# Performance work log

Measured on AMD Instinct MI355X. Metric: run time of the kernel, lower is better.

Reference implementation:

```python
import jax, jax.numpy as jnp
import numpy as np

B, S, P = 64, 1024, 1024
D_IN, D, OUT = 50, 300, 1024
LN_EPS = 1e-6  # custom LayerNorm in repo-style code (a_2/b_2, eps=1e-6)


def setup_inputs() -> dict:
    key = jax.random.key(0)
    ks = jax.random.split(key, 16)
    std = 1e-4  # matches torch .normal_(mean=0, std=0.0001)
    return {
        "x": jax.random.normal(ks[0], (B, S, D_IN), jnp.float32),
        "matrix_embed": jax.random.normal(ks[1], (D_IN, D), jnp.float32),
        "past": jax.random.normal(ks[2], (B, P, D_IN), jnp.float32),
        "w_pt": jax.random.normal(ks[3], (D_IN, D), jnp.float32) * std,
        "b_pt": jax.random.normal(ks[4], (1, D), jnp.float32) * std,
        "w_pg": jax.random.normal(ks[5], (D_IN, D), jnp.float32) * std,
        "b_pg": jax.random.normal(ks[6], (1, D), jnp.float32) * std,
        "w_ps": jax.random.normal(ks[7], (D_IN, D), jnp.float32) * std,
        "b_ps": jax.random.normal(ks[8], (1, D), jnp.float32) * std,
        "w_ex": jax.random.normal(ks[9], (D_IN, D), jnp.float32) * std,
        "b_ex": jax.random.normal(ks[10], (1, D), jnp.float32) * std,
        "ln_g": jnp.ones((D,), jnp.float32),
        "ln_b": jnp.zeros((D,), jnp.float32),
        "W1": jax.random.normal(ks[11], (D, D), jnp.float32) * 0.05,
        "b1": jnp.zeros((D,), jnp.float32),
        "W2": jax.random.normal(ks[12], (D, OUT), jnp.float32) * 0.05,
        "b2": jnp.zeros((OUT,), jnp.float32),
    }


def _layernorm(h, g, b):
    mu = jnp.mean(h, axis=-1, keepdims=True)
    var = jnp.mean(jnp.square(h - mu), axis=-1, keepdims=True)
    return g * (h - mu) / jnp.sqrt(var + LN_EPS) + b


def reference(x, matrix_embed, past, w_pt, b_pt, w_pg, b_pg, w_ps, b_ps,
              w_ex, b_ex, ln_g, ln_b, W1, b1, W2, b2):
    # token: [B,S,300]
    token = _layernorm(x @ matrix_embed, ln_g, ln_b)
    past_token = jnp.tanh(x @ w_pt + b_pt)          # [B,S,300]
    past_vector = jnp.tanh(past @ w_pg + b_pg)      # [B,P,300]
    past_gate = jax.nn.sigmoid(jnp.einsum('bsd,bpd->bsp', past_token, past_vector))
    past_state = jnp.tanh(past @ w_ps + b_ps)       # [B,P,300]
    pre_state = past_gate @ past_state              # [B,S,300]
    expose_vector = jnp.tanh(x @ w_ex + b_ex)       # [B,S,300]
    expose_gate = jax.nn.sigmoid(jnp.einsum('bsd,btd->bst', expose_vector, pre_state))
    filter_token = token + expose_gate @ pre_state  # [B,S,300]
    # output MLP (dropout is identity in eval mode)
    h = jax.nn.relu(filter_token @ W1 + b1)
    return h @ W2 + b2
```

## Files before the change

kernel.cpp:

```cpp
#include <hip/hip_runtime.h>
#include <hip/hip_bf16.h>
#include <math.h>

typedef __attribute__((ext_vector_type(8))) short bf16x8;
typedef __attribute__((ext_vector_type(4))) float f32x4;

__device__ inline float bf2f(short u) {
  union { float f; unsigned int i; } v;
  v.i = ((unsigned int)(unsigned short)u) << 16;
  return v.f;
}
__device__ inline short f2bf(float f) {
  union { float f; unsigned int i; } v; v.f = f;
  unsigned int r = v.i + 0x7fff + ((v.i >> 16) & 1);
  return (short)(r >> 16);
}

__global__ void pad_rows(const float* __restrict__ src, short* __restrict__ dst,
                         int C, int Cp, int total) {
  int i = blockIdx.x * 256 + threadIdx.x;
  if (i >= total) return;
  int r = i / Cp, c = i - r * Cp;
  dst[i] = f2bf(c < C ? src[(size_t)r * C + c] : 0.f);
}

__global__ void pad_T(const float* __restrict__ src, short* __restrict__ dst,
                      int K, int N, int Kp, int total) {
  int i = blockIdx.x * 256 + threadIdx.x;
  if (i >= total) return;
  int n = i / Kp, k = i - n * Kp;
  dst[i] = f2bf((k < K && n < N) ? src[(size_t)k * N + n] : 0.f);
}

__global__ __launch_bounds__(256) void transpose_pd(const short* __restrict__ in,
                                                    short* __restrict__ out) {
  __shared__ unsigned int T[64][32];
  const int b = blockIdx.z, p0 = blockIdx.x * 64, d0 = blockIdx.y * 64;
  const short* ib = in + (size_t)b * 1024 * 320;
  short* ob = out + (size_t)b * 320 * 1024;
  for (int i = threadIdx.x; i < 512; i += 256) {
    int p = i >> 3, g = i & 7;
    uint4 v = *(const uint4*)&ib[(size_t)(p0 + p) * 320 + d0 + g * 8];
    int s = p & 31;
    T[p][(4 * g + 0) ^ s] = v.x;
    T[p][(4 * g + 1) ^ s] = v.y;
    T[p][(4 * g + 2) ^ s] = v.z;
    T[p][(4 * g + 3) ^ s] = v.w;
  }
  __syncthreads();
  for (int i = threadIdx.x; i < 512; i += 256) {
    int d = i >> 3, g = i & 7;
    int w0 = d >> 1;
    __align__(16) unsigned short tmp[8];
#pragma unroll
    for (int j = 0; j < 8; ++j) {
      int p = g * 8 + j;
      unsigned int val = T[p][w0 ^ (p & 31)];
      tmp[j] = (d & 1) ? (unsigned short)(val >> 16) : (unsigned short)(val & 0xffff);
    }
    *(uint4*)&ob[(size_t)(d0 + d) * 1024 + p0 + g * 8] = *(const uint4*)tmp;
  }
}

template<int NT, int MODE>
__global__ __launch_bounds__(512) void gemm_ep(
    const short* __restrict__ A, const short* __restrict__ Bt, int K,
    const float* __restrict__ bias, int biasN,
    void* __restrict__ outp, int outStride)
{
  __shared__ __align__(16) short Bst[NT][40];
  const int tid = threadIdx.x;
  const int wave = tid >> 6, lane = tid & 63;
  const int m = lane & 15, quad = lane >> 4;
  const int row0 = blockIdx.x * 128 + wave * 16;
  const int n0 = blockIdx.y * NT;

  f32x4 zero = {0.f, 0.f, 0.f, 0.f};
  f32x4 acc[NT / 16];
#pragma unroll
  for (int i = 0; i < NT / 16; ++i) acc[i] = zero;

  const short* arow = A + (size_t)(row0 + m) * K;

  for (int k0 = 0; k0 < K; k0 += 32) {
    __syncthreads();
    for (int idx = tid; idx < NT * 4; idx += 512) {
      int n = idx >> 2, kc = (idx & 3) << 3;
      *(uint4*)&Bst[n][kc] = *(const uint4*)&Bt[(size_t)(n0 + n) * K + k0 + kc];
    }
    __syncthreads();
    bf16x8 af = *(const bf16x8*)(arow + k0 + quad * 8);
#pragma unroll
    for (int nt = 0; nt < NT / 16; ++nt) {
      bf16x8 bf = *(const bf16x8*)&Bst[nt * 16 + m][quad * 8];
      acc[nt] = __builtin_amdgcn_mfma_f32_16x16x32_bf16(af, bf, acc[nt], 0, 0, 0);
    }
  }

#pragma unroll
  for (int nt = 0; nt < NT / 16; ++nt) {
#pragma unroll
    for (int r = 0; r < 4; ++r) {
      int row = row0 + quad * 4 + r;
      int col = n0 + nt * 16 + m;
      float v = acc[nt][r];
      if (MODE != 0) v += (col < biasN) ? bias[col] : 0.f;
      if (MODE == 1) v = tanhf(v);
      if (MODE == 2) v = fmaxf(v, 0.f);
      if (MODE == 3)
        ((float*)outp)[(size_t)row * outStride + col] = v;
      else
        ((short*)outp)[(size_t)row * outStride + col] = f2bf(v);
    }
  }
}

__global__ __launch_bounds__(256) void ln_rows(short* __restrict__ tp,
                                               const float* __restrict__ g,
                                               const float* __restrict__ bb) {
  const int wave = threadIdx.x >> 6, lane = threadIdx.x & 63;
  const int row = blockIdx.x * 4 + wave;
  short* p = tp + (size_t)row * 320;
  float vals[5], s = 0.f, ss = 0.f;
#pragma unroll
  for (int i = 0; i < 5; ++i) {
    int c = lane + i * 64;
    float v = (c < 300) ? bf2f(p[c]) : 0.f;
    vals[i] = v; s += v; ss += v * v;
  }
#pragma unroll
  for (int off = 32; off > 0; off >>= 1) { s += __shfl_down(s, off); ss += __shfl_down(ss, off); }
  s = __shfl(s, 0); ss = __shfl(ss, 0);
  const float mu = s * (1.f / 300.f);
  const float rstd = rsqrtf(ss * (1.f / 300.f) - mu * mu + 1e-6f);
#pragma unroll
  for (int i = 0; i < 5; ++i) {
    int c = lane + i * 64;
    float v = (c < 300) ? (g[c] * (vals[i] - mu) * rstd + bb[c]) : 0.f;
    p[c] = f2bf(v);
  }
}

__global__ __launch_bounds__(512) void attn_v2(
    const short* __restrict__ Qm, const short* __restrict__ Km,
    const short* __restrict__ VT, const short* __restrict__ tokp,
    short* __restrict__ Outp)
{
  __shared__ __align__(16) short Ks[32][328];
  __shared__ __align__(16) short Vt[320][40];
  __shared__ __align__(16) short Ps[8][16][40];
  const int tid = threadIdx.x;
  const int wave = tid >> 6, lane = tid & 63;
  const int m = lane & 15, quad = lane >> 4;
  const int b = blockIdx.x;
  const int qrow0 = b * 1024 + blockIdx.y * 128 + wave * 16;
  const size_t kbase = (size_t)b * 1024 * 320;
  const short* vtb = VT + (size_t)b * 320 * 1024;

  bf16x8 qf[10];
#pragma unroll
  for (int c = 0; c < 10; ++c)
    qf[c] = *(const bf16x8*)&Qm[(size_t)(qrow0 + m) * 320 + c * 32 + quad * 8];

  f32x4 zero = {0.f, 0.f, 0.f, 0.f};
  f32x4 o[20];
#pragma unroll
  for (int i = 0; i < 20; ++i) o[i] = zero;

  for (int pt = 0; pt < 32; ++pt) {
    const int p0 = pt * 32;
    __syncthreads();
    for (int idx = tid; idx < 1280; idx += 512) {
      int p = idx / 40, g = idx - p * 40;
      *(uint4*)&Ks[p][g * 8] = *(const uint4*)&Km[kbase + (size_t)(p0 + p) * 320 + g * 8];
    }
    for (int idx = tid; idx < 1280; idx += 512) {
      int d = idx >> 2, g = idx & 3;
      *(uint4*)&Vt[d][g * 8] = *(const uint4*)&vtb[(size_t)d * 1024 + p0 + g * 8];
    }
    __syncthreads();

    f32x4 s0 = zero, s1 = zero;
#pragma unroll
    for (int c = 0; c < 10; ++c) {
      bf16x8 b0 = *(const bf16x8*)&Ks[m][c * 32 + quad * 8];
      bf16x8 b1 = *(const bf16x8*)&Ks[m + 16][c * 32 + quad * 8];
      s0 = __builtin_amdgcn_mfma_f32_16x16x32_bf16(qf[c], b0, s0, 0, 0, 0);
      s1 = __builtin_amdgcn_mfma_f32_16x16x32_bf16(qf[c], b1, s1, 0, 0, 0);
    }
#pragma unroll
    for (int r = 0; r < 4; ++r) {
      float v0 = 1.f / (1.f + __expf(-s0[r]));
      float v1 = 1.f / (1.f + __expf(-s1[r]));
      Ps[wave][quad * 4 + r][m] = f2bf(v0);
      Ps[wave][quad * 4 + r][m + 16] = f2bf(v1);
    }
    bf16x8 pa = *(const bf16x8*)&Ps[wave][m][quad * 8];
#pragma unroll
    for (int nt = 0; nt < 20; ++nt) {
      bf16x8 vb = *(const bf16x8*)&Vt[nt * 16 + m][quad * 8];
      o[nt] = __builtin_amdgcn_mfma_f32_16x16x32_bf16(pa, vb, o[nt], 0, 0, 0);
    }
  }

#pragma unroll
  for (int nt = 0; nt < 20; ++nt) {
#pragma unroll
    for (int r = 0; r < 4; ++r) {
      int row = qrow0 + quad * 4 + r;
      int col = nt * 16 + m;
      float v = o[nt][r];
      if (tokp) v += bf2f(tokp[(size_t)row * 320 + col]);
      Outp[(size_t)row * 320 + col] = f2bf(v);
    }
  }
}

extern "C" void kernel_launch(void* const* d_in, const int* in_sizes, int n_in,
                              void* d_out, int out_size, void* d_ws, size_t ws_size,
                              hipStream_t stream)
{
  const float* x    = (const float*)d_in[0];
  const float* me   = (const float*)d_in[1];
  const float* past = (const float*)d_in[2];
  const float* wpt  = (const float*)d_in[3];
  const float* bpt  = (const float*)d_in[4];
  const float* wpg  = (const float*)d_in[5];
  const float* bpg  = (const float*)d_in[6];
  const float* wps  = (const float*)d_in[7];
  const float* bps  = (const float*)d_in[8];
  const float* wex  = (const float*)d_in[9];
  const float* bex  = (const float*)d_in[10];
  const float* lng  = (const float*)d_in[11];
  const float* lnb  = (const float*)d_in[12];
  const float* W1   = (const float*)d_in[13];
  const float* b1   = (const float*)d_in[14];
  const float* W2   = (const float*)d_in[15];
  const float* b2   = (const float*)d_in[16];
  float* out = (float*)d_out;

  char* ws = (char*)d_ws;
  size_t off = 0;
  auto alloc = [&](size_t bytes) -> char* {
    char* p = ws + off; off += (bytes + 255) & ~(size_t)255; return p;
  };
  const size_t RB = 65536ull;
  short* xp    = (short*)alloc(RB * 64 * 2);
  short* pastp = (short*)alloc(RB * 64 * 2);
  short* wmeT  = (short*)alloc(320 * 64 * 2);
  short* wptT  = (short*)alloc(320 * 64 * 2);
  short* wpgT  = (short*)alloc(320 * 64 * 2);
  short* wpsT  = (short*)alloc(320 * 64 * 2);
  short* wexT  = (short*)alloc(320 * 64 * 2);
  short* w1T   = (short*)alloc(320 * 320 * 2);
  short* w2T   = (short*)alloc(1024ull * 320 * 2);
  short* buf0  = (short*)alloc(RB * 320 * 2);
  short* buf1  = (short*)alloc(RB * 320 * 2);
  short* buf2  = (short*)alloc(RB * 320 * 2);
  short* buf3  = (short*)alloc(RB * 320 * 2);
  short* vtbuf = (short*)alloc(RB * 320 * 2);

  {
    int total = 65536 * 64;
    pad_rows<<<dim3((total + 255) / 256), 256, 0, stream>>>(x, xp, 50, 64, total);
    pad_rows<<<dim3((total + 255) / 256), 256, 0, stream>>>(past, pastp, 50, 64, total);
  }
  {
    int t = 320 * 64;
    dim3 g((t + 255) / 256);
    pad_T<<<g, 256, 0, stream>>>(me,  wmeT, 50, 300, 64, t);
    pad_T<<<g, 256, 0, stream>>>(wpt, wptT, 50, 300, 64, t);
    pad_T<<<g, 256, 0, stream>>>(wpg, wpgT, 50, 300, 64, t);
    pad_T<<<g, 256, 0, stream>>>(wps, wpsT, 50, 300, 64, t);
    pad_T<<<g, 256, 0, stream>>>(wex, wexT, 50, 300, 64, t);
  }
  { int t = 320 * 320;  pad_T<<<(t + 255) / 256, 256, 0, stream>>>(W1, w1T, 300, 300, 320, t); }
  { int t = 1024 * 320; pad_T<<<(t + 255) / 256, 256, 0, stream>>>(W2, w2T, 300, 1024, 320, t); }

  dim3 g512(512, 1);
  dim3 tgrid(16, 5, 64);
  gemm_ep<320, 1><<<g512, 512, 0, stream>>>(xp,    wptT, 64, bpt, 300, buf0, 320);
  gemm_ep<320, 1><<<g512, 512, 0, stream>>>(pastp, wpgT, 64, bpg, 300, buf1, 320);
  gemm_ep<320, 1><<<g512, 512, 0, stream>>>(pastp, wpsT, 64, bps, 300, buf2, 320);
  transpose_pd<<<tgrid, 256, 0, stream>>>(buf2, vtbuf);

  attn_v2<<<dim3(64, 8), 512, 0, stream>>>(buf0, buf1, vtbuf, nullptr, buf3);

  gemm_ep<320, 0><<<g512, 512, 0, stream>>>(xp, wmeT, 64, nullptr, 0, buf1, 320);
  ln_rows<<<16384, 256, 0, stream>>>(buf1, lng, lnb);
  gemm_ep<320, 1><<<g512, 512, 0, stream>>>(xp, wexT, 64, bex, 300, buf2, 320);

  transpose_pd<<<tgrid, 256, 0, stream>>>(buf3, vtbuf);

  attn_v2<<<dim3(64, 8), 512, 0, stream>>>(buf2, buf3, vtbuf, buf1, buf0);

  gemm_ep<320, 2><<<g512, 512, 0, stream>>>(buf0, w1T, 320, b1, 300, buf3, 320);
  gemm_ep<256, 3><<<dim3(512, 4), 512, 0, stream>>>(buf3, w2T, 320, b2, 1024, out, 1024);
}
```

Before: 1.144 ms.

## Warp-specialize sigmoid-attention into QK and PV waves with double-buffered async LDS loads

Replaces the attention kernel with a warp-specialized version. Four waves compute QK^T scores and the sigmoid, and four waves do P@V on the previous tile. Global-to-LDS loads go through global_load_lds into double buffers, with an XOR swizzle on the K rows to avoid bank conflicts. The aim is to overlap load latency and the two matmul stages instead of running them serially with full syncs, at the cost of more LDS, explicit waitcnt barriers and a one-tile pipeline lag that adds correctness risk.

```diff
diff --git a/kernel.cpp b/kernel.cpp
--- a/kernel.cpp
+++ b/kernel.cpp
@@ -141,78 +141,154 @@
   }
 }
 
-__global__ __launch_bounds__(512) void attn_v2(
+__device__ inline void gload16(const short* g, short* l) {
+  __builtin_amdgcn_global_load_lds((const __attribute__((address_space(1))) void*)g,
+                                   (__attribute__((address_space(3))) void*)l, 16, 0, 0);
+}
+__device__ inline void block_sync() {
+  asm volatile("s_waitcnt vmcnt(0) lgkmcnt(0)" ::: "memory");
+  __builtin_amdgcn_s_barrier();
+  __builtin_amdgcn_sched_barrier(0);
+}
+
+__global__ __launch_bounds__(512, 2) void attn_v3(
     const short* __restrict__ Qm, const short* __restrict__ Km,
     const short* __restrict__ VT, const short* __restrict__ tokp,
     short* __restrict__ Outp)
 {
-  __shared__ __align__(16) short Ks[32][328];
-  __shared__ __align__(16) short Vt[320][40];
-  __shared__ __align__(16) short Ps[8][16][40];
+  __shared__ __align__(16) short KsL[2][10240];
+  __shared__ __align__(16) short VsL[2][10240];
+  __shared__ __align__(16) short PsL[2][5120];
+
   const int tid = threadIdx.x;
   const int wave = tid >> 6, lane = tid & 63;
   const int m = lane & 15, quad = lane >> 4;
   const int b = blockIdx.x;
-  const int qrow0 = b * 1024 + blockIdx.y * 128 + wave * 16;
+  const int qrow0 = b * 1024 + blockIdx.y * 128;
   const size_t kbase = (size_t)b * 1024 * 320;
   const short* vtb = VT + (size_t)b * 320 * 1024;
 
-  bf16x8 qf[10];
-#pragma unroll
-  for (int c = 0; c < 10; ++c)
-    qf[c] = *(const bf16x8*)&Qm[(size_t)(qrow0 + m) * 320 + c * 32 + quad * 8];
-
-  f32x4 zero = {0.f, 0.f, 0.f, 0.f};
-  f32x4 o[20];
-#pragma unroll
-  for (int i = 0; i < 20; ++i) o[i] = zero;
-
-  for (int pt = 0; pt < 32; ++pt) {
-    const int p0 = pt * 32;
-    __syncthreads();
-    for (int idx = tid; idx < 1280; idx += 512) {
-      int p = idx / 40, g = idx - p * 40;
-      *(uint4*)&Ks[p][g * 8] = *(const uint4*)&Km[kbase + (size_t)(p0 + p) * 320 + g * 8];
-    }
-    for (int idx = tid; idx < 1280; idx += 512) {
-      int d = idx >> 2, g = idx & 3;
-      *(uint4*)&Vt[d][g * 8] = *(const uint4*)&vtb[(size_t)d * 1024 + p0 + g * 8];
-    }
-    __syncthreads();
-
-    f32x4 s0 = zero, s1 = zero;
-#pragma unroll
-    for (int c = 0; c < 10; ++c) {
-      bf16x8 b0 = *(const bf16x8*)&Ks[m][c * 32 + quad * 8];
-      bf16x8 b1 = *(const bf16x8*)&Ks[m + 16][c * 32 + quad * 8];
-      s0 = __builtin_amdgcn_mfma_f32_16x16x32_bf16(qf[c], b0, s0, 0, 0, 0);
-      s1 = __builtin_amdgcn_mfma_f32_16x16x32_bf16(qf[c], b1, s1, 0, 0, 0);
-    }
-#pragma unroll
-    for (int r = 0; r < 4; ++r) {
-      float v0 = 1.f / (1.f + __expf(-s0[r]));
-      float v1 = 1.f / (1.f + __expf(-s1[r]));
-      Ps[wave][quad * 4 + r][m] = f2bf(v0);
-      Ps[wave][quad * 4 + r][m + 16] = f2bf(v1);
-    }
-    bf16x8 pa = *(const bf16x8*)&Ps[wave][m][quad * 8];
-#pragma unroll
-    for (int nt = 0; nt < 20; ++nt) {
-      bf16x8 vb = *(const bf16x8*)&Vt[nt * 16 + m][quad * 8];
-      o[nt] = __builtin_amdgcn_mfma_f32_16x16x32_bf16(pa, vb, o[nt], 0, 0, 0);
-    }
-  }
-
-#pragma unroll
-  for (int nt = 0; nt < 20; ++nt) {
-#pragma unroll
-    for (int r = 0; r < 4; ++r) {
-      int row = qrow0 + quad * 4 + r;
-      int col = nt * 16 + m;
-      float v = o[nt][r];
-      if (tokp) v += bf2f(tokp[(size_t)row * 320 + col]);
-      Outp[(size_t)row * 320 + col] = f2bf(v);
-    }
+  const short* sp[5];
+#pragma unroll
+  for (int j = 0; j < 5; ++j) {
+    int c = tid + j * 512;
+    if (c < 1280) {
+      int p = c / 40, ch = c - p * 40;
+      sp[j] = Km + kbase + (size_t)p * 320 + (ch ^ ((p & 1) << 2)) * 8;
+    } else {
+      int cv = c - 1280;
+      sp[j] = vtb + (size_t)(cv >> 2) * 1024 + (cv & 3) * 8;
+    }
+  }
+
+  auto stage = [&](int pt) {
+#pragma unroll
+    for (int j = 0; j < 5; ++j) {
+      int cb = j * 512 + (wave << 6);
+      if (cb < 1280) {
+        if (pt < 31)
+          gload16(sp[j] + (size_t)(pt + 1) * 10240, &KsL[(pt + 1) & 1][cb * 8]);
+      } else {
+        gload16(sp[j] + pt * 32, &VsL[pt & 1][(cb - 1280) * 8]);
+      }
+    }
+  };
+
+#pragma unroll
+  for (int j = 0; j < 3; ++j) {
+    int cb = j * 512 + (wave << 6);
+    if (cb < 1280) gload16(sp[j], &KsL[0][cb * 8]);
+  }
+  block_sync();
+
+  if (wave < 4) {
+    bf16x8 qf[2][10];
+    const short* qb = Qm + (size_t)(qrow0 + wave * 32 + m) * 320;
+#pragma unroll
+    for (int h = 0; h < 2; ++h)
+#pragma unroll
+      for (int c = 0; c < 10; ++c)
+        qf[h][c] = *(const bf16x8*)(qb + h * 5120 + c * 32 + quad * 8);
+    const int par = m & 1;
+
+    for (int pt = 0; pt < 32; ++pt) {
+      stage(pt);
+      const short* Kc = &KsL[pt & 1][0];
+      f32x4 s00 = {0.f, 0.f, 0.f, 0.f}, s01 = s00, s10 = s00, s11 = s00;
+      __builtin_amdgcn_s_setprio(1);
+#pragma unroll
+      for (int c = 0; c < 10; ++c) {
+        int cc = c ^ par;
+        bf16x8 b0 = *(const bf16x8*)&Kc[m * 320 + cc * 32 + quad * 8];
+        bf16x8 b1 = *(const bf16x8*)&Kc[(m + 16) * 320 + cc * 32 + quad * 8];
+        s00 = __builtin_amdgcn_mfma_f32_16x16x32_bf16(qf[0][c], b0, s00, 0, 0, 0);
+        s10 = __builtin_amdgcn_mfma_f32_16x16x32_bf16(qf[1][c], b0, s10, 0, 0, 0);
+        s01 = __builtin_amdgcn_mfma_f32_16x16x32_bf16(qf[0][c], b1, s01, 0, 0, 0);
+        s11 = __builtin_amdgcn_mfma_f32_16x16x32_bf16(qf[1][c], b1, s11, 0, 0, 0);
+      }
+      __builtin_amdgcn_s_setprio(0);
+      short* Pb = &PsL[pt & 1][0];
+#pragma unroll
+      for (int h = 0; h < 2; ++h) {
+        const int qt = wave * 2 + h;
+#pragma unroll
+        for (int g = 0; g < 2; ++g) {
+          f32x4 sv = h ? (g ? s11 : s10) : (g ? s01 : s00);
+#pragma unroll
+          for (int r = 0; r < 4; ++r) {
+            float v = 1.f / (1.f + __expf(-sv[r]));
+            Pb[qt * 640 + (quad * 4 + r) * 40 + g * 16 + m] = f2bf(v);
+          }
+        }
+      }
+      block_sync();
+    }
+  } else {
+    const int ds = wave - 4;
+    f32x4 zero = {0.f, 0.f, 0.f, 0.f};
+    f32x4 o[8][5];
+#pragma unroll
+    for (int i = 0; i < 8; ++i)
+#pragma unroll
+      for (int j = 0; j < 5; ++j) o[i][j] = zero;
+
+    auto pv_step = [&](int t) {
+      const short* Vc = &VsL[t & 1][0];
+      const short* Pr = &PsL[t & 1][0];
+      bf16x8 vb[5];
+#pragma unroll
+      for (int u = 0; u < 5; ++u)
+        vb[u] = *(const bf16x8*)&Vc[(ds * 80 + u * 16 + m) * 32 + quad * 8];
+      __builtin_amdgcn_s_setprio(1);
+#pragma unroll
+      for (int qt = 0; qt < 8; ++qt) {
+        bf16x8 pa = *(const bf16x8*)&Pr[qt * 640 + m * 40 + quad * 8];
+#pragma unroll
+        for (int u = 0; u < 5; ++u)
+          o[qt][u] = __builtin_amdgcn_mfma_f32_16x16x32_bf16(pa, vb[u], o[qt][u], 0, 0, 0);
+      }
+      __builtin_amdgcn_s_setprio(0);
+    };
+
+    for (int pt = 0; pt < 32; ++pt) {
+      stage(pt);
+      if (pt > 0) pv_step(pt - 1);
+      block_sync();
+    }
+    pv_step(31);
+
+#pragma unroll
+    for (int qt = 0; qt < 8; ++qt)
+#pragma unroll
+      for (int u = 0; u < 5; ++u)
+#pragma unroll
+        for (int r = 0; r < 4; ++r) {
+          const size_t row = (size_t)qrow0 + qt * 16 + quad * 4 + r;
+          const int col = ds * 80 + u * 16 + m;
+          float v = o[qt][u][r];
+          if (tokp) v += bf2f(tokp[row * 320 + col]);
+          Outp[row * 320 + col] = f2bf(v);
+        }
   }
 }
 
@@ -284,7 +360,7 @@
   gemm_ep<320, 1><<<g512, 512, 0, stream>>>(pastp, wpsT, 64, bps, 300, buf2, 320);
   transpose_pd<<<tgrid, 256, 0, stream>>>(buf2, vtbuf);
 
-  attn_v2<<<dim3(64, 8), 512, 0, stream>>>(buf0, buf1, vtbuf, nullptr, buf3);
+  attn_v3<<<dim3(64, 8), 512, 0, stream>>>(buf0, buf1, vtbuf, nullptr, buf3);
 
   gemm_ep<320, 0><<<g512, 512, 0, stream>>>(xp, wmeT, 64, nullptr, 0, buf1, 320);
   ln_rows<<<16384, 256, 0, stream>>>(buf1, lng, lnb);
@@ -292,7 +368,7 @@
 
   transpose_pd<<<tgrid, 256, 0, stream>>>(buf3, vtbuf);
 
-  attn_v2<<<dim3(64, 8), 512, 0, stream>>>(buf2, buf3, vtbuf, buf1, buf0);
+  attn_v3<<<dim3(64, 8), 512, 0, stream>>>(buf2, buf3, vtbuf, buf1, buf0);
 
   gemm_ep<320, 2><<<g512, 512, 0, stream>>>(buf0, w1T, 320, b1, 300, buf3, 320);
   gemm_ep<256, 3><<<dim3(512, 4), 512, 0, stream>>>(buf3, w2T, 320, b2, 1024, out, 1024);
```

Measured after the change: 1.092 ms. 1.05x faster.

## Double-buffer attention K/V tiles with direct global-to-LDS loads and register P transpose

Applied to the files above, without the earlier changes.

Rewrites the attention kernel to double-buffer K and V^T tiles in LDS, filled by global_load_lds so the next tile's load overlaps the current tile's MFMAs, with a single barrier per iteration. LDS layouts use XOR swizzling in place of padding to avoid bank conflicts. The score MFMA is computed transposed, and the sigmoid probabilities are repacked into the A operand in registers via permlane32_swap and ds_swizzle, skipping the LDS round trip. Launch bounds now request two blocks per CU, which limits registers per thread and may cause spills.

```diff
diff --git a/kernel.cpp b/kernel.cpp
--- a/kernel.cpp
+++ b/kernel.cpp
@@ -141,79 +141,137 @@
   }
 }
 
-__global__ __launch_bounds__(512) void attn_v2(
+__device__ inline void gload16(const short* g, short* l) {
+  __builtin_amdgcn_global_load_lds((const __attribute__((address_space(1))) void*)g,
+                                   (__attribute__((address_space(3))) void*)l, 16, 0, 0);
+}
+__device__ inline void block_sync() {
+  asm volatile("s_waitcnt vmcnt(0) lgkmcnt(0)" ::: "memory");
+  __builtin_amdgcn_s_barrier();
+  __builtin_amdgcn_sched_barrier(0);
+}
+
+__global__ __launch_bounds__(512, 2) void attn_v6(
     const short* __restrict__ Qm, const short* __restrict__ Km,
     const short* __restrict__ VT, const short* __restrict__ tokp,
     short* __restrict__ Outp)
 {
-  __shared__ __align__(16) short Ks[32][328];
-  __shared__ __align__(16) short Vt[320][40];
-  __shared__ __align__(16) short Ps[8][16][40];
+  __shared__ __align__(16) short KsL[2][10240];
+  __shared__ __align__(16) short VsL[2][10240];
+
   const int tid = threadIdx.x;
   const int wave = tid >> 6, lane = tid & 63;
   const int m = lane & 15, quad = lane >> 4;
   const int b = blockIdx.x;
-  const int qrow0 = b * 1024 + blockIdx.y * 128 + wave * 16;
+  const int qrow0 = b * 1024 + blockIdx.y * 128;
   const size_t kbase = (size_t)b * 1024 * 320;
   const short* vtb = VT + (size_t)b * 320 * 1024;
 
+  const short* src[5];
+  int dst[5];
+#pragma unroll
+  for (int j = 0; j < 5; ++j) {
+    int c = j * 512 + tid;
+    if (c < 1280) {
+      int p = c / 40, ch = c - p * 40;
+      src[j] = Km + kbase + (size_t)p * 320 + ((ch ^ (p & 7)) << 3);
+      dst[j] = c << 3;
+    } else {
+      int cv = c - 1280;
+      int d = cv >> 2, ch = cv & 3;
+      src[j] = vtb + (size_t)d * 1024 + ((ch ^ (d & 3)) << 3);
+      dst[j] = cv << 3;
+    }
+  }
+  const bool j2K = (wave < 4);
+
+  auto stage = [&](int pt) {
+    const int bb = pt & 1;
+    gload16(src[0] + (size_t)pt * 10240, &KsL[bb][dst[0]]);
+    gload16(src[1] + (size_t)pt * 10240, &KsL[bb][dst[1]]);
+    if (j2K) gload16(src[2] + (size_t)pt * 10240, &KsL[bb][dst[2]]);
+    else     gload16(src[2] + (size_t)pt * 32,    &VsL[bb][dst[2]]);
+    gload16(src[3] + (size_t)pt * 32, &VsL[bb][dst[3]]);
+    gload16(src[4] + (size_t)pt * 32, &VsL[bb][dst[4]]);
+  };
+
   bf16x8 qf[10];
+  const short* qb = Qm + (size_t)(qrow0 + wave * 16 + m) * 320;
 #pragma unroll
   for (int c = 0; c < 10; ++c)
-    qf[c] = *(const bf16x8*)&Qm[(size_t)(qrow0 + m) * 320 + c * 32 + quad * 8];
+    qf[c] = *(const bf16x8*)(qb + c * 32 + quad * 8);
 
   f32x4 zero = {0.f, 0.f, 0.f, 0.f};
   f32x4 o[20];
 #pragma unroll
   for (int i = 0; i < 20; ++i) o[i] = zero;
 
+  const int vch = (quad ^ (m & 3)) << 3;
+  const unsigned oddq = (unsigned)(quad & 1);
+
+  stage(0);
+  block_sync();
+
   for (int pt = 0; pt < 32; ++pt) {
-    const int p0 = pt * 32;
-    __syncthreads();
-    for (int idx = tid; idx < 1280; idx += 512) {
-      int p = idx / 40, g = idx - p * 40;
-      *(uint4*)&Ks[p][g * 8] = *(const uint4*)&Km[kbase + (size_t)(p0 + p) * 320 + g * 8];
-    }
-    for (int idx = tid; idx < 1280; idx += 512) {
-      int d = idx >> 2, g = idx & 3;
-      *(uint4*)&Vt[d][g * 8] = *(const uint4*)&vtb[(size_t)d * 1024 + p0 + g * 8];
-    }
-    __syncthreads();
-
-    f32x4 s0 = zero, s1 = zero;
+    if (pt < 31) stage(pt + 1);
+    const short* Kc = &KsL[pt & 1][0];
+    const short* Vc = &VsL[pt & 1][0];
+
+    f32x4 sl = zero, sh = zero;
 #pragma unroll
     for (int c = 0; c < 10; ++c) {
-      bf16x8 b0 = *(const bf16x8*)&Ks[m][c * 32 + quad * 8];
-      bf16x8 b1 = *(const bf16x8*)&Ks[m + 16][c * 32 + quad * 8];
-      s0 = __builtin_amdgcn_mfma_f32_16x16x32_bf16(qf[c], b0, s0, 0, 0, 0);
-      s1 = __builtin_amdgcn_mfma_f32_16x16x32_bf16(qf[c], b1, s1, 0, 0, 0);
-    }
+      int ch0 = ((4 * c + quad) ^ (m & 7)) << 3;
+      bf16x8 k0 = *(const bf16x8*)&Kc[m * 320 + ch0];
+      bf16x8 k1 = *(const bf16x8*)&Kc[(m + 16) * 320 + ch0];
+      sl = __builtin_amdgcn_mfma_f32_16x16x32_bf16(k0, qf[c], sl, 0, 0, 0);
+      sh = __builtin_amdgcn_mfma_f32_16x16x32_bf16(k1, qf[c], sh, 0, 0, 0);
+    }
+
+    float e0[4], e1[4];
 #pragma unroll
     for (int r = 0; r < 4; ++r) {
-      float v0 = 1.f / (1.f + __expf(-s0[r]));
-      float v1 = 1.f / (1.f + __expf(-s1[r]));
-      Ps[wave][quad * 4 + r][m] = f2bf(v0);
-      Ps[wave][quad * 4 + r][m + 16] = f2bf(v1);
-    }
-    bf16x8 pa = *(const bf16x8*)&Ps[wave][m][quad * 8];
-#pragma unroll
-    for (int nt = 0; nt < 20; ++nt) {
-      bf16x8 vb = *(const bf16x8*)&Vt[nt * 16 + m][quad * 8];
-      o[nt] = __builtin_amdgcn_mfma_f32_16x16x32_bf16(pa, vb, o[nt], 0, 0, 0);
-    }
-  }
-
-#pragma unroll
-  for (int nt = 0; nt < 20; ++nt) {
+      e0[r] = 1.f / (1.f + __expf(-sl[r]));
+      e1[r] = 1.f / (1.f + __expf(-sh[r]));
+    }
+    int w0, w1, w2, w3;
+    asm("v_cvt_pk_bf16_f32 %0, %1, %2" : "=v"(w0) : "v"(e0[0]), "v"(e0[1]));
+    asm("v_cvt_pk_bf16_f32 %0, %1, %2" : "=v"(w1) : "v"(e0[2]), "v"(e0[3]));
+    asm("v_cvt_pk_bf16_f32 %0, %1, %2" : "=v"(w2) : "v"(e1[0]), "v"(e1[1]));
+    asm("v_cvt_pk_bf16_f32 %0, %1, %2" : "=v"(w3) : "v"(e1[2]), "v"(e1[3]));
+
+    int x0 = w0, y0 = w2, x1 = w1, y1 = w3;
+    asm volatile("v_permlane32_swap_b32 %0, %1" : "+v"(x0), "+v"(y0));
+    asm volatile("v_permlane32_swap_b32 %0, %1" : "+v"(x1), "+v"(y1));
+    int sx0 = __builtin_amdgcn_ds_swizzle(x0, 0x401f);
+    int sy0 = __builtin_amdgcn_ds_swizzle(y0, 0x401f);
+    int sx1 = __builtin_amdgcn_ds_swizzle(x1, 0x401f);
+    int sy1 = __builtin_amdgcn_ds_swizzle(y1, 0x401f);
+    union { int i[4]; bf16x8 v; } pu;
+    pu.i[0] = oddq ? sy0 : x0;
+    pu.i[1] = oddq ? sy1 : x1;
+    pu.i[2] = oddq ? y0 : sx0;
+    pu.i[3] = oddq ? y1 : sx1;
+    bf16x8 pa = pu.v;
+
+#pragma unroll
+    for (int dt = 0; dt < 20; ++dt) {
+      bf16x8 vb = *(const bf16x8*)&Vc[(dt * 16 + m) * 32 + vch];
+      o[dt] = __builtin_amdgcn_mfma_f32_16x16x32_bf16(pa, vb, o[dt], 0, 0, 0);
+    }
+
+    block_sync();
+  }
+
+#pragma unroll
+  for (int dt = 0; dt < 20; ++dt)
 #pragma unroll
     for (int r = 0; r < 4; ++r) {
-      int row = qrow0 + quad * 4 + r;
-      int col = nt * 16 + m;
-      float v = o[nt][r];
-      if (tokp) v += bf2f(tokp[(size_t)row * 320 + col]);
-      Outp[(size_t)row * 320 + col] = f2bf(v);
-    }
-  }
+      const size_t row = (size_t)qrow0 + wave * 16 + quad * 4 + r;
+      const int col = dt * 16 + m;
+      float val = o[dt][r];
+      if (tokp) val += bf2f(tokp[row * 320 + col]);
+      Outp[row * 320 + col] = f2bf(val);
+    }
 }
 
 extern "C" void kernel_launch(void* const* d_in, const int* in_sizes, int n_in,
@@ -284,7 +342,7 @@
   gemm_ep<320, 1><<<g512, 512, 0, stream>>>(pastp, wpsT, 64, bps, 300, buf2, 320);
   transpose_pd<<<tgrid, 256, 0, stream>>>(buf2, vtbuf);
 
-  attn_v2<<<dim3(64, 8), 512, 0, stream>>>(buf0, buf1, vtbuf, nullptr, buf3);
+  attn_v6<<<dim3(64, 8), 512, 0, stream>>>(buf0, buf1, vtbuf, nullptr, buf3);
 
   gemm_ep<320, 0><<<g512, 512, 0, stream>>>(xp, wmeT, 64, nullptr, 0, buf1, 320);
   ln_rows<<<16384, 256, 0, stream>>>(buf1, lng, lnb);
@@ -292,7 +350,7 @@
 
   transpose_pd<<<tgrid, 256, 0, stream>>>(buf3, vtbuf);
 
-  attn_v2<<<dim3(64, 8), 512, 0, stream>>>(buf2, buf3, vtbuf, buf1, buf0);
+  attn_v6<<<dim3(64, 8), 512, 0, stream>>>(buf2, buf3, vtbuf, buf1, buf0);
 
   gemm_ep<320, 2><<<g512, 512, 0, stream>>>(buf0, w1T, 320, b1, 300, buf3, 320);
   gemm_ep<256, 3><<<dim3(512, 4), 512, 0, stream>>>(buf3, w2T, 320, b2, 1024, out, 1024);
```

After: 0.9999 ms. 1.14x faster.
